# Performance work log

Hardware: AMD Instinct MI355X
Metric: run time of the kernel (lower is better)

Reference implementation:

```python
import jax, jax.numpy as jnp
import numpy as np

# Module hyperparameters (init_kwargs)
NUM_EXPERTS = 8
HIDDEN = 1024
CAP_FACTORS = [0.5, 0.75, 1.0, 1.0, 1.25, 1.25, 1.5, 1.5]


def setup_inputs() -> dict:
    key = jax.random.key(0)
    k1, k2, k3 = jax.random.split(key, 3)
    G, T = 4, 2048
    token_inputs = jax.random.normal(k1, (G, T, HIDDEN), dtype=jnp.float32)
    # RouterWeights = nn.Linear(hidden, num_experts, bias=True)
    W = jax.random.normal(k2, (HIDDEN, NUM_EXPERTS), dtype=jnp.float32) * (1.0 / np.sqrt(HIDDEN))
    b = jax.random.normal(k3, (NUM_EXPERTS,), dtype=jnp.float32) * 0.01
    return {"token_inputs": token_inputs, "W": W, "b": b, "expert_capacity": 256}


def reference(token_inputs, W, b, expert_capacity):
    # token_inputs: [G, T, H]; jitter_noise=0 so no jitter; ignore_padding_tokens=False
    G, T, _ = token_inputs.shape
    logits = jnp.einsum("gth,he->gte", token_inputs, W) + b  # [G, T, E]
    probs = jax.nn.softmax(logits, axis=-1)
    # router z-loss: mean(logsumexp(logits, -1)^2)
    z_loss = jnp.mean(jax.nn.logsumexp(logits, axis=-1) ** 2)

    capacities = [int(expert_capacity * f) for f in CAP_FACTORS]
    max_cap = max(capacities)

    dispatch_slices = []  # each [G, T, max_cap] int32
    combine_slices = []   # each [G, T, max_cap] float32
    for e, cap in enumerate(capacities):
        gate, idx = jax.lax.top_k(probs[:, :, e], cap)  # [G, cap]
        # one_hot(idx, T): [G, cap, T] -> transpose to [G, T, cap]
        oh = jax.nn.one_hot(idx, T, dtype=jnp.int32).transpose(0, 2, 1)  # [G, T, cap]
        oh = jnp.pad(oh, ((0, 0), (0, 0), (0, max_cap - cap)))
        dispatch_slices.append(oh)
        # combine: gate broadcast over tokens dim (as in original code)
        comb = jnp.broadcast_to(gate[:, None, :], (G, T, cap))  # [G, T, cap]
        comb = jnp.pad(comb, ((0, 0), (0, 0), (0, max_cap - cap)))
        combine_slices.append(comb)

    dispatch_mask = jnp.stack(dispatch_slices, axis=1)  # [G, E, T, max_cap]
    combine_array = jnp.stack(combine_slices, axis=1).astype(jnp.float32)  # [G, E, T, max_cap]
    auxiliary_loss = jnp.float32(0.0)
    return dispatch_mask, combine_array, auxiliary_loss, z_loss
```

## Files before the change

kernel.cpp:

```cpp
#include <hip/hip_runtime.h>
#include <hip/hip_bf16.h>
#include <math.h>

#define G 4
#define T 2048
#define H 1024
#define E 8
#define LB 2048
#define ZB1 1024
#define RB 256
#define ZB2 1024

typedef float f4 __attribute__((ext_vector_type(4)));
typedef unsigned long long u64;
typedef unsigned long long u64v2 __attribute__((ext_vector_type(2)));

__global__ __launch_bounds__(256) void k1_logits_zero_init(
    const float* __restrict__ x, const float* __restrict__ W,
    const float* __restrict__ b, u64* __restrict__ keys,
    float* __restrict__ lse2, float* __restrict__ out,
    float* __restrict__ gate, int* __restrict__ idx, unsigned n4d,
    int max_cap) {
  unsigned bid = blockIdx.x;
  unsigned tid = threadIdx.x;

  if (bid < LB) {
    int wave = (int)(bid * 4 + (tid >> 6));
    int lane = tid & 63;
    const float* xr = x + (size_t)wave * H;

    double acc0 = 0, acc1 = 0, acc2 = 0, acc3 = 0;
    double acc4 = 0, acc5 = 0, acc6 = 0, acc7 = 0;
#pragma unroll
    for (int j = 0; j < 4; ++j) {
      int hbase = j * 256 + lane * 4;
      f4 xv = *(const f4*)(xr + hbase);
#pragma unroll
      for (int k = 0; k < 4; ++k) {
        const float* wr = W + (size_t)(hbase + k) * 8;
        f4 w0 = *(const f4*)(wr);
        f4 w1 = *(const f4*)(wr + 4);
        double xd = (double)xv[k];
        acc0 += xd * (double)w0[0];
        acc1 += xd * (double)w0[1];
        acc2 += xd * (double)w0[2];
        acc3 += xd * (double)w0[3];
        acc4 += xd * (double)w1[0];
        acc5 += xd * (double)w1[1];
        acc6 += xd * (double)w1[2];
        acc7 += xd * (double)w1[3];
      }
    }
#pragma unroll
    for (int off = 32; off >= 1; off >>= 1) {
      acc0 += __shfl_xor(acc0, off);
      acc1 += __shfl_xor(acc1, off);
      acc2 += __shfl_xor(acc2, off);
      acc3 += __shfl_xor(acc3, off);
      acc4 += __shfl_xor(acc4, off);
      acc5 += __shfl_xor(acc5, off);
      acc6 += __shfl_xor(acc6, off);
      acc7 += __shfl_xor(acc7, off);
    }
    if (lane == 0) {
      double l0 = acc0 + (double)b[0], l1 = acc1 + (double)b[1];
      double l2 = acc2 + (double)b[2], l3 = acc3 + (double)b[3];
      double l4 = acc4 + (double)b[4], l5 = acc5 + (double)b[5];
      double l6 = acc6 + (double)b[6], l7 = acc7 + (double)b[7];
      double m = fmax(fmax(fmax(l0, l1), fmax(l2, l3)),
                      fmax(fmax(l4, l5), fmax(l6, l7)));
      double pr[8];
      pr[0] = exp(l0 - m);
      pr[1] = exp(l1 - m);
      pr[2] = exp(l2 - m);
      pr[3] = exp(l3 - m);
      pr[4] = exp(l4 - m);
      pr[5] = exp(l5 - m);
      pr[6] = exp(l6 - m);
      pr[7] = exp(l7 - m);
      double s = ((pr[0] + pr[1]) + (pr[2] + pr[3])) +
                 ((pr[4] + pr[5]) + (pr[6] + pr[7]));
      double inv = 1.0 / s;
      int g = wave >> 11;
      int t = wave & (T - 1);
      u64* kb = keys + (size_t)g * 8 * T + t;
#pragma unroll
      for (int e = 0; e < 8; ++e) {
        float pf = (float)(pr[e] * inv);
        kb[(size_t)e * T] =
            ((u64)__float_as_uint(pf) << 32) | (unsigned)(~t);
      }
      double lse = m + log(s);
      lse2[wave] = (float)(lse * lse);
    }
  } else if (bid < LB + ZB1) {
    f4* outD = (f4*)out;
    f4 z = {0.0f, 0.0f, 0.0f, 0.0f};
    unsigned half = n4d >> 1;
    unsigned stride = ZB1 * 256u;
    for (unsigned i = (bid - LB) * 256u + tid; i < half; i += stride)
      outD[i] = z;
  } else {
    unsigned s = (bid - LB - ZB1) * 256u + tid;
    if (s < (unsigned)(G * E * max_cap)) {
      gate[s] = 0.0f;
      idx[s] = -1;
    }
  }
}

__global__ __launch_bounds__(256) void k2_rank_zero(
    const u64* __restrict__ keys, float* __restrict__ gate,
    int* __restrict__ idx, float* __restrict__ out, unsigned n4d, int max_cap,
    int ec) {
  __shared__ u64 lk[T];
  unsigned bid = blockIdx.x;
  unsigned tid = threadIdx.x;

  if (bid < RB) {
    int ge = (int)(bid >> 3);
    int chunk = (int)(bid & 7);
    const u64* kcol = keys + (size_t)ge * T;
    for (int t = tid; t < T; t += 256) lk[t] = kcol[t];
    __syncthreads();

    int myt = chunk * 256 + (int)tid;
    u64 mine = lk[myt];

    const u64v2* k2p = (const u64v2*)lk;
    int r0 = 0, r1 = 0, r2 = 0, r3 = 0;
    u64v2 p0 = k2p[0], p1 = k2p[1], p2 = k2p[2], p3 = k2p[3];
    for (int j = 4; j < T / 2; j += 4) {
      u64v2 q0 = k2p[j], q1 = k2p[j + 1], q2 = k2p[j + 2], q3 = k2p[j + 3];
      r0 += (int)(p0.x > mine) + (int)(p0.y > mine);
      r1 += (int)(p1.x > mine) + (int)(p1.y > mine);
      r2 += (int)(p2.x > mine) + (int)(p2.y > mine);
      r3 += (int)(p3.x > mine) + (int)(p3.y > mine);
      p0 = q0;
      p1 = q1;
      p2 = q2;
      p3 = q3;
    }
    r0 += (int)(p0.x > mine) + (int)(p0.y > mine);
    r1 += (int)(p1.x > mine) + (int)(p1.y > mine);
    r2 += (int)(p2.x > mine) + (int)(p2.y > mine);
    r3 += (int)(p3.x > mine) + (int)(p3.y > mine);
    int rank = (r0 + r1) + (r2 + r3);

    const double factors[8] = {0.5, 0.75, 1.0, 1.0, 1.25, 1.25, 1.5, 1.5};
    int cap = (int)((double)ec * factors[ge & 7]);
    if (rank < cap) {
      gate[(size_t)ge * max_cap + rank] =
          __uint_as_float((unsigned)(mine >> 32));
      idx[(size_t)ge * max_cap + rank] = myt;
    }
  } else {
    f4* outD = (f4*)out;
    f4 z = {0.0f, 0.0f, 0.0f, 0.0f};
    unsigned half = n4d >> 1;
    unsigned stride = ZB2 * 256u;
    for (unsigned i = half + (bid - RB) * 256u + tid; i < n4d; i += stride)
      outD[i] = z;
  }
}

template <int MC4S>
__global__ __launch_bounds__(256) void scatter_and_combine(
    const float* __restrict__ gate, const int* __restrict__ idx,
    const float* __restrict__ lse2, float* __restrict__ out, unsigned n4d,
    unsigned mc4_rt, int max_cap, unsigned scb) {
  const unsigned mc4 = MC4S ? (unsigned)MC4S : mc4_rt;
  unsigned tid = threadIdx.x;
  unsigned bid = blockIdx.x;

  if (bid == 0) {
    __shared__ double red[256];
    double s = 0.0;
    for (int i = tid; i < G * T; i += 256) s += (double)lse2[i];
    red[tid] = s;
    __syncthreads();
    for (int off = 128; off > 0; off >>= 1) {
      if ((int)tid < off) red[tid] += red[tid + off];
      __syncthreads();
    }
    if (tid == 0) {
      size_t ne = (size_t)n4d * 4;
      out[2 * ne] = 0.0f;
      out[2 * ne + 1] = (float)(red[0] / (double)(G * T));
    }
    return;
  }
  if (bid <= scb) {
    unsigned s = (bid - 1) * 256u + tid;
    if (s < (unsigned)(G * E) * (unsigned)max_cap) {
      unsigned ge = s / (unsigned)max_cap;
      unsigned c = s - ge * (unsigned)max_cap;
      int t = idx[s];
      if (t >= 0) out[((size_t)ge * T + t) * (unsigned)max_cap + c] = 1.0f;
    }
    return;
  }

  f4* outC = (f4*)out + n4d;
  const f4* gate4 = (const f4*)gate;
  unsigned fb = bid - 1 - scb;
  unsigned nfb = gridDim.x - 1 - scb;
  unsigned stride = nfb * 256u;
  for (unsigned i = fb * 256u + tid; i < n4d; i += stride) {
    unsigned c4 = i % mc4;
    unsigned rem = i / mc4;
    unsigned ge = rem >> 11;
    outC[i] = gate4[ge * mc4 + c4];
  }
}

extern "C" void kernel_launch(void* const* d_in, const int* in_sizes, int n_in,
                              void* d_out, int out_size, void* d_ws,
                              size_t ws_size, hipStream_t stream) {
  const float* x = (const float*)d_in[0];
  const float* W = (const float*)d_in[1];
  const float* b = (const float*)d_in[2];

  long long body = (long long)out_size - 2;
  int max_cap = (int)(body / (2LL * G * E * T));
  if (max_cap <= 0) return;
  int ec = (2 * max_cap) / 3;

  u64* keys = (u64*)d_ws;
  float* lse2 = (float*)(keys + (size_t)G * E * T);
  float* gate = lse2 + (size_t)G * T;
  int* idx = (int*)(gate + (size_t)G * E * max_cap);

  unsigned n4d = (unsigned)((long long)G * E * T * max_cap / 4);
  unsigned scb = (unsigned)((G * E * max_cap + 255) / 256);

  k1_logits_zero_init<<<LB + ZB1 + scb, 256, 0, stream>>>(
      x, W, b, keys, lse2, (float*)d_out, gate, idx, n4d, max_cap);
  k2_rank_zero<<<RB + ZB2, 256, 0, stream>>>(keys, gate, idx, (float*)d_out,
                                             n4d, max_cap, ec);

  int blocks = 6144;
  if (max_cap == 384) {
    scatter_and_combine<96><<<blocks, 256, 0, stream>>>(
        gate, idx, lse2, (float*)d_out, n4d, 96u, max_cap, scb);
  } else {
    scatter_and_combine<0><<<blocks, 256, 0, stream>>>(
        gate, idx, lse2, (float*)d_out, n4d, (unsigned)(max_cap / 4), max_cap,
        scb);
  }
}
```

Baseline: 83.66 us.

## Move full dispatch zeroing to first kernel and scatter ones directly from rank kernel

```diff
diff --git a/kernel.cpp b/kernel.cpp
--- a/kernel.cpp
+++ b/kernel.cpp
@@ -6,169 +6,157 @@
 #define T 2048
 #define H 1024
 #define E 8
-#define LB 2048
-#define ZB1 1024
-#define RB 256
-#define ZB2 1024
+#define ZK1 2048
+#define LGB 2048
+#define PB 48
 
 typedef float f4 __attribute__((ext_vector_type(4)));
 typedef unsigned long long u64;
 typedef unsigned long long u64v2 __attribute__((ext_vector_type(2)));
 
-__global__ __launch_bounds__(256) void k1_logits_zero_init(
+__global__ __launch_bounds__(256) void k1_zero_logits(
     const float* __restrict__ x, const float* __restrict__ W,
     const float* __restrict__ b, u64* __restrict__ keys,
-    float* __restrict__ lse2, float* __restrict__ out,
-    float* __restrict__ gate, int* __restrict__ idx, unsigned n4d,
-    int max_cap) {
+    float* __restrict__ lse2, float* __restrict__ gate,
+    float* __restrict__ out, unsigned n4d, int max_cap) {
   unsigned bid = blockIdx.x;
   unsigned tid = threadIdx.x;
 
-  if (bid < LB) {
-    int wave = (int)(bid * 4 + (tid >> 6));
-    int lane = tid & 63;
-    const float* xr = x + (size_t)wave * H;
-
-    double acc0 = 0, acc1 = 0, acc2 = 0, acc3 = 0;
-    double acc4 = 0, acc5 = 0, acc6 = 0, acc7 = 0;
-#pragma unroll
-    for (int j = 0; j < 4; ++j) {
-      int hbase = j * 256 + lane * 4;
-      f4 xv = *(const f4*)(xr + hbase);
-#pragma unroll
-      for (int k = 0; k < 4; ++k) {
-        const float* wr = W + (size_t)(hbase + k) * 8;
-        f4 w0 = *(const f4*)(wr);
-        f4 w1 = *(const f4*)(wr + 4);
-        double xd = (double)xv[k];
-        acc0 += xd * (double)w0[0];
-        acc1 += xd * (double)w0[1];
-        acc2 += xd * (double)w0[2];
-        acc3 += xd * (double)w0[3];
-        acc4 += xd * (double)w1[0];
-        acc5 += xd * (double)w1[1];
-        acc6 += xd * (double)w1[2];
-        acc7 += xd * (double)w1[3];
-      }
-    }
-#pragma unroll
-    for (int off = 32; off >= 1; off >>= 1) {
-      acc0 += __shfl_xor(acc0, off);
-      acc1 += __shfl_xor(acc1, off);
-      acc2 += __shfl_xor(acc2, off);
-      acc3 += __shfl_xor(acc3, off);
-      acc4 += __shfl_xor(acc4, off);
-      acc5 += __shfl_xor(acc5, off);
-      acc6 += __shfl_xor(acc6, off);
-      acc7 += __shfl_xor(acc7, off);
-    }
-    if (lane == 0) {
-      double l0 = acc0 + (double)b[0], l1 = acc1 + (double)b[1];
-      double l2 = acc2 + (double)b[2], l3 = acc3 + (double)b[3];
-      double l4 = acc4 + (double)b[4], l5 = acc5 + (double)b[5];
-      double l6 = acc6 + (double)b[6], l7 = acc7 + (double)b[7];
-      double m = fmax(fmax(fmax(l0, l1), fmax(l2, l3)),
-                      fmax(fmax(l4, l5), fmax(l6, l7)));
-      double pr[8];
-      pr[0] = exp(l0 - m);
-      pr[1] = exp(l1 - m);
-      pr[2] = exp(l2 - m);
-      pr[3] = exp(l3 - m);
-      pr[4] = exp(l4 - m);
-      pr[5] = exp(l5 - m);
-      pr[6] = exp(l6 - m);
-      pr[7] = exp(l7 - m);
-      double s = ((pr[0] + pr[1]) + (pr[2] + pr[3])) +
-                 ((pr[4] + pr[5]) + (pr[6] + pr[7]));
-      double inv = 1.0 / s;
-      int g = wave >> 11;
-      int t = wave & (T - 1);
-      u64* kb = keys + (size_t)g * 8 * T + t;
-#pragma unroll
-      for (int e = 0; e < 8; ++e) {
-        float pf = (float)(pr[e] * inv);
-        kb[(size_t)e * T] =
-            ((u64)__float_as_uint(pf) << 32) | (unsigned)(~t);
-      }
-      double lse = m + log(s);
-      lse2[wave] = (float)(lse * lse);
-    }
-  } else if (bid < LB + ZB1) {
+  if (bid < ZK1) {
     f4* outD = (f4*)out;
     f4 z = {0.0f, 0.0f, 0.0f, 0.0f};
-    unsigned half = n4d >> 1;
-    unsigned stride = ZB1 * 256u;
-    for (unsigned i = (bid - LB) * 256u + tid; i < half; i += stride)
-      outD[i] = z;
-  } else {
-    unsigned s = (bid - LB - ZB1) * 256u + tid;
-    if (s < (unsigned)(G * E * max_cap)) {
-      gate[s] = 0.0f;
-      idx[s] = -1;
+    unsigned stride = ZK1 * 256u;
+    for (unsigned i = bid * 256u + tid; i < n4d; i += stride) outD[i] = z;
+    return;
+  }
+  if (bid >= ZK1 + LGB) {
+    unsigned s = (bid - ZK1 - LGB) * 256u + tid;
+    if (s < (unsigned)(G * E * max_cap)) gate[s] = 0.0f;
+    return;
+  }
+
+  int wave = (int)((bid - ZK1) * 4 + (tid >> 6));
+  int lane = (int)(tid & 63);
+  const float* xr = x + (size_t)wave * H;
+
+  double acc0 = 0, acc1 = 0, acc2 = 0, acc3 = 0;
+  double acc4 = 0, acc5 = 0, acc6 = 0, acc7 = 0;
+#pragma unroll
+  for (int j = 0; j < 4; ++j) {
+    int hbase = j * 256 + lane * 4;
+    f4 xv = *(const f4*)(xr + hbase);
+#pragma unroll
+    for (int k = 0; k < 4; ++k) {
+      const float* wr = W + (size_t)(hbase + k) * 8;
+      f4 w0 = *(const f4*)(wr);
+      f4 w1 = *(const f4*)(wr + 4);
+      double xd = (double)xv[k];
+      acc0 += xd * (double)w0[0];
+      acc1 += xd * (double)w0[1];
+      acc2 += xd * (double)w0[2];
+      acc3 += xd * (double)w0[3];
+      acc4 += xd * (double)w1[0];
+      acc5 += xd * (double)w1[1];
+      acc6 += xd * (double)w1[2];
+      acc7 += xd * (double)w1[3];
     }
   }
-}
-
-__global__ __launch_bounds__(256) void k2_rank_zero(
+#pragma unroll
+  for (int off = 32; off >= 1; off >>= 1) {
+    acc0 += __shfl_xor(acc0, off);
+    acc1 += __shfl_xor(acc1, off);
+    acc2 += __shfl_xor(acc2, off);
+    acc3 += __shfl_xor(acc3, off);
+    acc4 += __shfl_xor(acc4, off);
+    acc5 += __shfl_xor(acc5, off);
+    acc6 += __shfl_xor(acc6, off);
+    acc7 += __shfl_xor(acc7, off);
+  }
+  double l0 = acc0 + (double)b[0], l1 = acc1 + (double)b[1];
+  double l2 = acc2 + (double)b[2], l3 = acc3 + (double)b[3];
+  double l4 = acc4 + (double)b[4], l5 = acc5 + (double)b[5];
+  double l6 = acc6 + (double)b[6], l7 = acc7 + (double)b[7];
+  double m = fmax(fmax(fmax(l0, l1), fmax(l2, l3)),
+                  fmax(fmax(l4, l5), fmax(l6, l7)));
+  double la = (lane & 1) ? l1 : l0;
+  double lb = (lane & 1) ? l3 : l2;
+  double lc = (lane & 1) ? l5 : l4;
+  double ld = (lane & 1) ? l7 : l6;
+  double le = (lane & 2) ? lb : la;
+  double lf = (lane & 2) ? ld : lc;
+  double lsel = (lane & 4) ? lf : le;
+
+  double pe = exp(lsel - m);
+  double s = pe;
+  s += __shfl_xor(s, 1);
+  s += __shfl_xor(s, 2);
+  s += __shfl_xor(s, 4);
+  double inv = 1.0 / s;
+  float pf = (float)(pe * inv);
+
+  int g = wave >> 11;
+  int t = wave & (T - 1);
+  if (lane < 8) {
+    keys[((size_t)g * 8 + lane) * T + t] =
+        ((u64)__float_as_uint(pf) << 32) | (unsigned)(~t);
+  }
+  if (lane == 0) {
+    double lse = m + log(s);
+    lse2[wave] = (float)(lse * lse);
+  }
+}
+
+__global__ __launch_bounds__(256) void k2_rank(
     const u64* __restrict__ keys, float* __restrict__ gate,
-    int* __restrict__ idx, float* __restrict__ out, unsigned n4d, int max_cap,
-    int ec) {
+    float* __restrict__ out, int max_cap, int ec) {
   __shared__ u64 lk[T];
   unsigned bid = blockIdx.x;
   unsigned tid = threadIdx.x;
-
-  if (bid < RB) {
-    int ge = (int)(bid >> 3);
-    int chunk = (int)(bid & 7);
-    const u64* kcol = keys + (size_t)ge * T;
-    for (int t = tid; t < T; t += 256) lk[t] = kcol[t];
-    __syncthreads();
-
-    int myt = chunk * 256 + (int)tid;
-    u64 mine = lk[myt];
-
-    const u64v2* k2p = (const u64v2*)lk;
-    int r0 = 0, r1 = 0, r2 = 0, r3 = 0;
-    u64v2 p0 = k2p[0], p1 = k2p[1], p2 = k2p[2], p3 = k2p[3];
-    for (int j = 4; j < T / 2; j += 4) {
-      u64v2 q0 = k2p[j], q1 = k2p[j + 1], q2 = k2p[j + 2], q3 = k2p[j + 3];
-      r0 += (int)(p0.x > mine) + (int)(p0.y > mine);
-      r1 += (int)(p1.x > mine) + (int)(p1.y > mine);
-      r2 += (int)(p2.x > mine) + (int)(p2.y > mine);
-      r3 += (int)(p3.x > mine) + (int)(p3.y > mine);
-      p0 = q0;
-      p1 = q1;
-      p2 = q2;
-      p3 = q3;
-    }
+  int ge = (int)(bid >> 3);
+  int chunk = (int)(bid & 7);
+
+  {
+    const u64v2* src = (const u64v2*)(keys + (size_t)ge * T);
+    u64v2* dst = (u64v2*)lk;
+    for (int i = tid; i < T / 2; i += 256) dst[i] = src[i];
+  }
+  __syncthreads();
+
+  int myt = chunk * 256 + (int)tid;
+  u64 mine = lk[myt];
+
+  const u64v2* k2p = (const u64v2*)lk;
+  int r0 = 0, r1 = 0, r2 = 0, r3 = 0;
+  u64v2 p0 = k2p[0], p1 = k2p[1], p2 = k2p[2], p3 = k2p[3];
+  for (int j = 4; j < T / 2; j += 4) {
+    u64v2 q0 = k2p[j], q1 = k2p[j + 1], q2 = k2p[j + 2], q3 = k2p[j + 3];
     r0 += (int)(p0.x > mine) + (int)(p0.y > mine);
     r1 += (int)(p1.x > mine) + (int)(p1.y > mine);
     r2 += (int)(p2.x > mine) + (int)(p2.y > mine);
     r3 += (int)(p3.x > mine) + (int)(p3.y > mine);
-    int rank = (r0 + r1) + (r2 + r3);
-
-    const double factors[8] = {0.5, 0.75, 1.0, 1.0, 1.25, 1.25, 1.5, 1.5};
-    int cap = (int)((double)ec * factors[ge & 7]);
-    if (rank < cap) {
-      gate[(size_t)ge * max_cap + rank] =
-          __uint_as_float((unsigned)(mine >> 32));
-      idx[(size_t)ge * max_cap + rank] = myt;
-    }
-  } else {
-    f4* outD = (f4*)out;
-    f4 z = {0.0f, 0.0f, 0.0f, 0.0f};
-    unsigned half = n4d >> 1;
-    unsigned stride = ZB2 * 256u;
-    for (unsigned i = half + (bid - RB) * 256u + tid; i < n4d; i += stride)
-      outD[i] = z;
+    p0 = q0;
+    p1 = q1;
+    p2 = q2;
+    p3 = q3;
+  }
+  r0 += (int)(p0.x > mine) + (int)(p0.y > mine);
+  r1 += (int)(p1.x > mine) + (int)(p1.y > mine);
+  r2 += (int)(p2.x > mine) + (int)(p2.y > mine);
+  r3 += (int)(p3.x > mine) + (int)(p3.y > mine);
+  int rank = (r0 + r1) + (r2 + r3);
+
+  const double factors[8] = {0.5, 0.75, 1.0, 1.0, 1.25, 1.25, 1.5, 1.5};
+  int cap = (int)((double)ec * factors[ge & 7]);
+  if (rank < cap) {
+    gate[(size_t)ge * max_cap + rank] = __uint_as_float((unsigned)(mine >> 32));
+    out[((size_t)ge * T + myt) * (unsigned)max_cap + rank] = 1.0f;
   }
 }
 
 template <int MC4S>
-__global__ __launch_bounds__(256) void scatter_and_combine(
-    const float* __restrict__ gate, const int* __restrict__ idx,
-    const float* __restrict__ lse2, float* __restrict__ out, unsigned n4d,
-    unsigned mc4_rt, int max_cap, unsigned scb) {
+__global__ __launch_bounds__(256) void k3_combine(
+    const float* __restrict__ gate, const float* __restrict__ lse2,
+    float* __restrict__ out, unsigned n4d, unsigned mc4_rt) {
   const unsigned mc4 = MC4S ? (unsigned)MC4S : mc4_rt;
   unsigned tid = threadIdx.x;
   unsigned bid = blockIdx.x;
@@ -190,26 +178,15 @@
     }
     return;
   }
-  if (bid <= scb) {
-    unsigned s = (bid - 1) * 256u + tid;
-    if (s < (unsigned)(G * E) * (unsigned)max_cap) {
-      unsigned ge = s / (unsigned)max_cap;
-      unsigned c = s - ge * (unsigned)max_cap;
-      int t = idx[s];
-      if (t >= 0) out[((size_t)ge * T + t) * (unsigned)max_cap + c] = 1.0f;
-    }
-    return;
-  }
 
   f4* outC = (f4*)out + n4d;
   const f4* gate4 = (const f4*)gate;
-  unsigned fb = bid - 1 - scb;
-  unsigned nfb = gridDim.x - 1 - scb;
+  unsigned fb = bid - 1;
+  unsigned nfb = gridDim.x - 1;
   unsigned stride = nfb * 256u;
   for (unsigned i = fb * 256u + tid; i < n4d; i += stride) {
     unsigned c4 = i % mc4;
-    unsigned rem = i / mc4;
-    unsigned ge = rem >> 11;
+    unsigned ge = (i / mc4) >> 11;
     outC[i] = gate4[ge * mc4 + c4];
   }
 }
@@ -229,23 +206,19 @@
   u64* keys = (u64*)d_ws;
   float* lse2 = (float*)(keys + (size_t)G * E * T);
   float* gate = lse2 + (size_t)G * T;
-  int* idx = (int*)(gate + (size_t)G * E * max_cap);
 
   unsigned n4d = (unsigned)((long long)G * E * T * max_cap / 4);
-  unsigned scb = (unsigned)((G * E * max_cap + 255) / 256);
-
-  k1_logits_zero_init<<<LB + ZB1 + scb, 256, 0, stream>>>(
-      x, W, b, keys, lse2, (float*)d_out, gate, idx, n4d, max_cap);
-  k2_rank_zero<<<RB + ZB2, 256, 0, stream>>>(keys, gate, idx, (float*)d_out,
-                                             n4d, max_cap, ec);
+
+  k1_zero_logits<<<ZK1 + LGB + PB, 256, 0, stream>>>(
+      x, W, b, keys, lse2, gate, (float*)d_out, n4d, max_cap);
+  k2_rank<<<256, 256, 0, stream>>>(keys, gate, (float*)d_out, max_cap, ec);
 
   int blocks = 6144;
   if (max_cap == 384) {
-    scatter_and_combine<96><<<blocks, 256, 0, stream>>>(
-        gate, idx, lse2, (float*)d_out, n4d, 96u, max_cap, scb);
+    k3_combine<96><<<blocks, 256, 0, stream>>>(gate, lse2, (float*)d_out, n4d,
+                                               96u);
   } else {
-    scatter_and_combine<0><<<blocks, 256, 0, stream>>>(
-        gate, idx, lse2, (float*)d_out, n4d, (unsigned)(max_cap / 4), max_cap,
-        scb);
-  }
-}
+    k3_combine<0><<<blocks, 256, 0, stream>>>(gate, lse2, (float*)d_out, n4d,
+                                              (unsigned)(max_cap / 4));
+  }
+}
```

Result: slower. 88.52 us (+5.8%).
